# Performance work log

Measured on AMD Instinct MI355X. Metric: run time of the kernel, lower is better.

## Reference

```python
import jax, jax.numpy as jnp
import numpy as np

NB, NX, NY, NU, NQ = 16384, 256, 128, 128, 128


def setup_inputs() -> dict:
    key = jax.random.key(0)
    ks = jax.random.split(key, 14)
    sx = 1.0 / np.sqrt(NX)
    su = 1.0 / np.sqrt(NU)
    sq = 1.0 / np.sqrt(NQ)
    return {
        "x": jax.random.normal(ks[0], (NB, NX), jnp.float32),
        "u": jax.random.normal(ks[1], (NB, NU), jnp.float32),
        "F": jax.random.normal(ks[2], (NX, NX), jnp.float32) * sx,
        "B1": jax.random.normal(ks[3], (NX, NQ), jnp.float32) * sq,
        "B2": jax.random.normal(ks[4], (NX, NU), jnp.float32) * su,
        "C1": jax.random.normal(ks[5], (NQ, NX), jnp.float32) * sx,
        "C2": jax.random.normal(ks[6], (NY, NX), jnp.float32) * sx,
        "D11": jax.random.normal(ks[7], (NQ, NQ), jnp.float32) * sq,
        "D12": jax.random.normal(ks[8], (NQ, NU), jnp.float32) * su,
        "D21": jax.random.normal(ks[9], (NY, NQ), jnp.float32) * sq,
        "D22": jax.random.normal(ks[10], (NY, NU), jnp.float32) * su,
        # E must be invertible (torch code takes torch.inverse(E))
        "E": jnp.eye(NX, dtype=jnp.float32) + 0.1 * sx * jax.random.normal(ks[11], (NX, NX), jnp.float32),
        # Lambda must be nonzero on the diagonal (divided by in the solve)
        "Lambda_vec": 1.0 + jax.random.uniform(ks[12], (NQ, 1), jnp.float32),
        "bv": 0.1 * jax.random.normal(ks[13], (NQ, 1), jnp.float32),
    }


def _solve_w(x, u, C1, D11, D12, Lambda_vec, bv):
    # Sequential forward substitution: v_k = (x@C1[k] + w@D11[k] + u@D12[k] + bv[k]) / Lambda[k,k]
    # w[:,j] for j >= k is zero at step k, so only the strictly-lower part of D11 contributes,
    # exactly matching the torch loop semantics.
    nq = C1.shape[0]
    base = x @ C1.T + u @ D12.T + bv[:, 0]  # (nb, nq), w-independent part
    lam = Lambda_vec[:, 0]                   # (nq,)
    w0 = jnp.zeros((x.shape[0], nq), x.dtype)

    def step(w, k):
        vk = (base[:, k] + w @ D11[k]) / lam[k]  # (nb,)
        return w.at[:, k].set(jnp.tanh(vk)), None

    w, _ = jax.lax.scan(step, w0, jnp.arange(nq))
    return w


def reference(x, u, F, B1, B2, C1, C2, D11, D12, D21, D22, E, Lambda_vec, bv):
    w = _solve_w(x, u, C1, D11, D12, Lambda_vec, bv)
    E_inv = jnp.linalg.inv(E)
    dx = x @ (E_inv @ F).T + w @ (E_inv @ B1).T + u @ (E_inv @ B2).T
    y = x @ C2.T + w @ D21.T + u @ D22.T  # feedthrough=True
    return dx, y
```

## Files before the change

kernel.cpp:

```cpp
#include <hip/hip_runtime.h>
#include <hip/hip_bf16.h>
#include <cstddef>

#define NBATCH 16384
#define NX 256
#define NY 128
#define NU 128
#define NQ 128

#define WS_A2     131072
#define WS_A4     196608
#define WS_P2     327680
#define WS_P4     393216
#define WS_WDX    524288
#define WS_BASE   655360
#define WS_W      2752512
#define WS_WCH    4849664
#define WS_WCL    4947968
#define WS_WBH    5046272
#define WS_WBL    5070848
#define WS_D11S   5095424

typedef __attribute__((ext_vector_type(8))) short bf8_t;
typedef __attribute__((ext_vector_type(4))) float f4_t;

#define C2LOG2E 2.8853900817779268f

__device__ __forceinline__ void gload_lds16(const void* g, void* l) {
  __builtin_amdgcn_global_load_lds(
      (const __attribute__((address_space(1))) unsigned int*)g,
      (__attribute__((address_space(3))) unsigned int*)l, 16, 0, 0);
}

__device__ __forceinline__ void splitbf(float a, unsigned short& h, unsigned short& l) {
  __hip_bfloat16 hb = __float2bfloat16(a);
  float hf = __bfloat162float(hb);
  __hip_bfloat16 lb = __float2bfloat16(a - hf);
  h = __builtin_bit_cast(unsigned short, hb);
  l = __builtin_bit_cast(unsigned short, lb);
}

__global__ __launch_bounds__(256) void k_smallmm(const float* __restrict__ A,
                                                 const float* __restrict__ B,
                                                 const float* __restrict__ X,
                                                 float* __restrict__ C,
                                                 int modeA, int modeB, int modeX) {
  __shared__ float As[32][36];
  __shared__ float Bs[32][36];
  int tid = threadIdx.x;
  int tx = tid & 15, ty = tid >> 4;
  int r0 = blockIdx.x * 32, c0 = blockIdx.y * 32;
  int lr = tid >> 3, lc = (tid & 7) * 4;
  float acc00 = 0.f, acc01 = 0.f, acc10 = 0.f, acc11 = 0.f;
  for (int k0 = 0; k0 < 256; k0 += 32) {
    float4 a4 = *(const float4*)&A[(size_t)(r0 + lr) * 256 + k0 + lc];
    float4 b4 = *(const float4*)&B[(size_t)(k0 + lr) * 256 + c0 + lc];
    if (modeA) {
      float av[4] = {a4.x, a4.y, a4.z, a4.w};
#pragma unroll
      for (int q = 0; q < 4; ++q) {
        float d = (r0 + lr == k0 + lc + q) ? 1.0f : 0.0f;
        av[q] = (modeA == 1) ? d - av[q] : 2.0f * d - av[q];
      }
      a4.x = av[0]; a4.y = av[1]; a4.z = av[2]; a4.w = av[3];
    }
    if (modeB) {
      float bvv[4] = {b4.x, b4.y, b4.z, b4.w};
#pragma unroll
      for (int q = 0; q < 4; ++q) {
        float d = (k0 + lr == c0 + lc + q) ? 1.0f : 0.0f;
        bvv[q] = (modeB == 1) ? d - bvv[q] : 2.0f * d - bvv[q];
      }
      b4.x = bvv[0]; b4.y = bvv[1]; b4.z = bvv[2]; b4.w = bvv[3];
    }
    __syncthreads();
    As[lr][lc+0] = a4.x; As[lr][lc+1] = a4.y; As[lr][lc+2] = a4.z; As[lr][lc+3] = a4.w;
    Bs[lr][lc+0] = b4.x; Bs[lr][lc+1] = b4.y; Bs[lr][lc+2] = b4.z; Bs[lr][lc+3] = b4.w;
    __syncthreads();
#pragma unroll
    for (int kk = 0; kk < 32; ++kk) {
      float a0 = As[ty*2+0][kk], a1 = As[ty*2+1][kk];
      float b0 = Bs[kk][tx*2+0], b1 = Bs[kk][tx*2+1];
      acc00 += a0*b0; acc01 += a0*b1; acc10 += a1*b0; acc11 += a1*b1;
    }
  }
  int r = r0 + ty*2, c = c0 + tx*2;
  if (modeX) {
#pragma unroll
    for (int i = 0; i < 2; ++i)
#pragma unroll
      for (int j = 0; j < 2; ++j) {
        float xv = X[(size_t)(r+i)*256 + c+j];
        float d = (r+i == c+j) ? 1.0f : 0.0f;
        float add = (modeX == 1) ? xv : 2.0f * d - xv;
        if (i==0 && j==0) acc00 += add;
        if (i==0 && j==1) acc01 += add;
        if (i==1 && j==0) acc10 += add;
        if (i==1 && j==1) acc11 += add;
      }
  }
  C[(size_t)r*256 + c]       = acc00; C[(size_t)r*256 + c+1]     = acc01;
  C[(size_t)(r+1)*256 + c]   = acc10; C[(size_t)(r+1)*256 + c+1] = acc11;
}

__global__ __launch_bounds__(256) void k_wdx(const float* __restrict__ P,
                                             const float* __restrict__ F,
                                             const float* __restrict__ B1,
                                             const float* __restrict__ B2,
                                             float* __restrict__ Wdx) {
  __shared__ float As[32][36];
  __shared__ float Bs[32][36];
  int tid = threadIdx.x;
  int tx = tid & 15, ty = tid >> 4;
  int r0 = blockIdx.x * 32, c0 = blockIdx.y * 32;
  const float* B; int ldb, cb;
  if (c0 < 256)      { B = F;  ldb = 256; cb = c0; }
  else if (c0 < 384) { B = B1; ldb = 128; cb = c0 - 256; }
  else               { B = B2; ldb = 128; cb = c0 - 384; }
  int lr = tid >> 3, lc = (tid & 7) * 4;
  float acc00 = 0.f, acc01 = 0.f, acc10 = 0.f, acc11 = 0.f;
  for (int k0 = 0; k0 < 256; k0 += 32) {
    float4 a4 = *(const float4*)&P[(size_t)(r0 + lr) * 256 + k0 + lc];
    float4 b4 = *(const float4*)&B[(size_t)(k0 + lr) * ldb + cb + lc];
    __syncthreads();
    As[lr][lc+0] = a4.x; As[lr][lc+1] = a4.y; As[lr][lc+2] = a4.z; As[lr][lc+3] = a4.w;
    Bs[lr][lc+0] = b4.x; Bs[lr][lc+1] = b4.y; Bs[lr][lc+2] = b4.z; Bs[lr][lc+3] = b4.w;
    __syncthreads();
#pragma unroll
    for (int kk = 0; kk < 32; ++kk) {
      float a0 = As[ty*2+0][kk], a1 = As[ty*2+1][kk];
      float b0 = Bs[kk][tx*2+0], b1 = Bs[kk][tx*2+1];
      acc00 += a0*b0; acc01 += a0*b1; acc10 += a1*b0; acc11 += a1*b1;
    }
  }
  int r = r0 + ty*2, c = c0 + tx*2;
  Wdx[(size_t)r*512 + c]       = acc00; Wdx[(size_t)r*512 + c+1]     = acc01;
  Wdx[(size_t)(r+1)*512 + c]   = acc10; Wdx[(size_t)(r+1)*512 + c+1] = acc11;
}

__global__ __launch_bounds__(256) void k_wprep(const float* __restrict__ Wdx,
                                               const float* __restrict__ C2,
                                               const float* __restrict__ D21,
                                               const float* __restrict__ D22,
                                               const float* __restrict__ C1,
                                               const float* __restrict__ D12,
                                               const float* __restrict__ D11,
                                               const float* __restrict__ Lam,
                                               ushort* __restrict__ Wh,
                                               ushort* __restrict__ Wl,
                                               ushort* __restrict__ Wbh,
                                               ushort* __restrict__ Wbl,
                                               float* __restrict__ D11s) {
  int i = blockIdx.x * 256 + threadIdx.x;
  if (i < 384 * 512) {
    int n = i >> 9, k = i & 511;
    float v;
    if (n < 256) v = Wdx[(size_t)n * 512 + k];
    else {
      int nn = n - 256;
      if (k < 256)      v = C2[(size_t)nn * 256 + k];
      else if (k < 384) v = D21[(size_t)nn * 128 + (k - 256)];
      else              v = D22[(size_t)nn * 128 + (k - 384)];
    }
    unsigned short h, l; splitbf(v, h, l);
    Wh[i] = h; Wl[i] = l;
  } else if (i < 384 * 512 + 128 * 384) {
    int j = i - 384 * 512;
    int n = j / 384, k = j - n * 384;
    float v = (k < 256) ? C1[(size_t)n * 256 + k] : D12[(size_t)n * 128 + (k - 256)];
    unsigned short h, l; splitbf(v, h, l);
    Wbh[j] = h; Wbl[j] = l;
  } else if (i < 384 * 512 + 128 * 384 + 128 * 128) {
    int j2 = i - (384 * 512 + 128 * 384);
    int jr = j2 >> 7;
    D11s[j2] = D11[j2] * (C2LOG2E / Lam[jr]);
  } else if (i < 384 * 512 + 128 * 384 + 128 * 128 + 128) {
    int i3 = i - (384 * 512 + 128 * 384 + 128 * 128);
    D11s[128 * 128 + i3] = C2LOG2E / Lam[i3];
  }
}

template <int KTOT, bool FINAL>
__global__ __launch_bounds__(256) void k_gemm2(const float* __restrict__ x,
                                               const float* __restrict__ u,
                                               const float* __restrict__ w,
                                               const ushort* __restrict__ Wh,
                                               const ushort* __restrict__ Wl,
                                               const float* __restrict__ bv,
                                               float* __restrict__ out) {
  __shared__ __align__(16) ushort sA[128 * 64];
  __shared__ __align__(16) ushort sB[64 * 64];
  const int tid  = threadIdx.x;
  const int lane = tid & 63, wav = tid >> 6;
  const int wm = wav >> 1, wn = wav & 1;
  const int row0 = blockIdx.x * 128;
  const int n0   = blockIdx.y * 64;
  const int fr = lane & 15, fc = lane >> 4;

  const int arow_l = tid >> 3;
  const int akb    = (tid & 7) * 4;

  f4_t acc[4][2];
#pragma unroll
  for (int i = 0; i < 4; ++i)
#pragma unroll
    for (int j = 0; j < 2; ++j) acc[i][j] = f4_t{0.f, 0.f, 0.f, 0.f};

  float4 ar[4];
#define LOAD_A(K0)                                                    \
  {                                                                   \
    int kseg = (K0) + akb;                                            \
    const float* ap0;                                                 \
    _Pragma("unroll")                                                 \
    for (int j = 0; j < 4; ++j) {                                     \
      size_t gr = (size_t)(row0 + j * 32 + arow_l);                   \
      if (FINAL) {                                                    \
        if (kseg < 256)      ap0 = x + gr * 256 + kseg;               \
        else if (kseg < 384) ap0 = w + gr * 128 + (kseg - 256);       \
        else                 ap0 = u + gr * 128 + (kseg - 384);       \
      } else {                                                        \
        if (kseg < 256)      ap0 = x + gr * 256 + kseg;               \
        else                 ap0 = u + gr * 128 + (kseg - 256);       \
      }                                                               \
      ar[j] = *(const float4*)ap0;                                    \
    }                                                                 \
  }

  const int NK = KTOT / 32;
  LOAD_A(0);

  for (int ks = 0; ks < NK; ++ks) {
    const int k0 = ks * 32;
    __syncthreads();

#pragma unroll
    for (int j = 0; j < 4; ++j) {
      int r = j * 32 + arow_l;
      unsigned short h0,l0,h1,l1,h2,l2,h3,l3;
      splitbf(ar[j].x, h0, l0); splitbf(ar[j].y, h1, l1);
      splitbf(ar[j].z, h2, l2); splitbf(ar[j].w, h3, l3);
      uint2 hv, lv;
      hv.x = (unsigned)h0 | ((unsigned)h1 << 16); hv.y = (unsigned)h2 | ((unsigned)h3 << 16);
      lv.x = (unsigned)l0 | ((unsigned)l1 << 16); lv.y = (unsigned)l2 | ((unsigned)l3 << 16);
      int ch   = (tid & 7) >> 1;
      int hoff = (tid & 1) * 8;
      char* rb = (char*)&sA[r * 64];
      *(uint2*)(rb + (((ch    ) ^ (r & 7)) << 4) + hoff) = hv;
      *(uint2*)(rb + (((ch + 4) ^ (r & 7)) << 4) + hoff) = lv;
    }

#pragma unroll
    for (int i = 0; i < 2; ++i) {
      int rbase = wav * 16 + i * 8;
      int nloc  = rbase + (lane >> 3);
      int c     = lane & 7;
      int g     = c ^ (nloc & 7);
      const ushort* src = (g < 4)
          ? (Wh + (size_t)(n0 + nloc) * KTOT + k0 + g * 8)
          : (Wl + (size_t)(n0 + nloc) * KTOT + k0 + (g - 4) * 8);
      gload_lds16(src, &sB[rbase * 64]);
    }

    {
      int kpre = (ks + 1 < NK) ? k0 + 32 : k0;
      LOAD_A(kpre);
    }
    asm volatile("s_waitcnt vmcnt(4)" ::: "memory");
    __syncthreads();

    bf8_t ah[4], al[4], bh[2], bl[2];
#pragma unroll
    for (int ms = 0; ms < 4; ++ms) {
      int r = wm * 64 + ms * 16 + fr;
      char* rb = (char*)&sA[r * 64];
      ah[ms] = *(const bf8_t*)(rb + (((fc    ) ^ (r & 7)) << 4));
      al[ms] = *(const bf8_t*)(rb + (((fc + 4) ^ (r & 7)) << 4));
    }
#pragma unroll
    for (int ns = 0; ns < 2; ++ns) {
      int n = wn * 32 + ns * 16 + fr;
      char* rb = (char*)&sB[n * 64];
      bh[ns] = *(const bf8_t*)(rb + (((fc    ) ^ (n & 7)) << 4));
      bl[ns] = *(const bf8_t*)(rb + (((fc + 4) ^ (n & 7)) << 4));
    }
#pragma unroll
    for (int ns = 0; ns < 2; ++ns)
#pragma unroll
      for (int ms = 0; ms < 4; ++ms) {
        acc[ms][ns] = __builtin_amdgcn_mfma_f32_16x16x32_bf16(ah[ms], bh[ns], acc[ms][ns], 0, 0, 0);
        acc[ms][ns] = __builtin_amdgcn_mfma_f32_16x16x32_bf16(ah[ms], bl[ns], acc[ms][ns], 0, 0, 0);
        acc[ms][ns] = __builtin_amdgcn_mfma_f32_16x16x32_bf16(al[ms], bh[ns], acc[ms][ns], 0, 0, 0);
      }
  }
#undef LOAD_A

#pragma unroll
  for (int ms = 0; ms < 4; ++ms) {
#pragma unroll
    for (int ns = 0; ns < 2; ++ns) {
#pragma unroll
      for (int j = 0; j < 4; ++j) {
        int m = row0 + wm * 64 + ms * 16 + fc * 4 + j;
        int n = n0 + wn * 32 + ns * 16 + fr;
        float v = acc[ms][ns][j];
        if (FINAL) {
          if (n0 < 256) out[(size_t)m * 256 + n] = v;
          else          out[(size_t)NBATCH * 256 + (size_t)m * 128 + (n - 256)] = v;
        } else {
          out[(size_t)m * 128 + n] = v + bv[n];
        }
      }
    }
  }
}

__device__ __forceinline__ float rdlane(float v, int l) {
  return __builtin_bit_cast(float, __builtin_amdgcn_readlane(__builtin_bit_cast(int, v), l));
}

#define WR 4
__global__ __launch_bounds__(256, 4) void k_wsolve(const float* __restrict__ baseo,
                                                   const float* __restrict__ D11s,
                                                   float* __restrict__ wout) {
  int tid = threadIdx.x;
  int lane = tid & 63, wave = tid >> 6;
  size_t rowbase = (size_t)blockIdx.x * (4 * WR) + (size_t)wave * WR;
  const float* drow0 = D11s + (size_t)lane * 128;
  const float* drow1 = D11s + (size_t)(64 + lane) * 128;
  const float* cvec  = D11s + 128 * 128;

  float t0[WR], t1[WR], w0[WR], w1[WR];
  float c0 = cvec[lane];
  float c1 = cvec[64 + lane];
#pragma unroll
  for (int r = 0; r < WR; ++r) {
    t0[r] = baseo[(rowbase + r) * 128 + lane] * c0;
    t1[r] = baseo[(rowbase + r) * 128 + 64 + lane] * c1;
    w0[r] = 0.f; w1[r] = 0.f;
  }
  float d0 = drow0[0];
  float d1 = drow1[0];
  for (int k = 0; k < 64; ++k) {
    int kn = k + 1;
    float nd0 = (kn < 64) ? drow0[kn] : 0.f;
    float nd1 = drow1[kn];
#pragma unroll
    for (int r = 0; r < WR; ++r) {
      float tk = rdlane(t0[r], k);
      float e  = __builtin_amdgcn_exp2f(tk);
      float wk = 1.0f - 2.0f * __builtin_amdgcn_rcpf(e + 1.0f);
      t0[r] += wk * d0;
      t1[r] += wk * d1;
      if (lane == k) w0[r] = wk;
    }
    d0 = nd0; d1 = nd1;
  }
  for (int k = 64; k < 128; ++k) {
    int kn = k + 1;
    float nd1 = (kn < 128) ? drow1[kn] : 0.f;
#pragma unroll
    for (int r = 0; r < WR; ++r) {
      float tk = rdlane(t1[r], k - 64);
      float e  = __builtin_amdgcn_exp2f(tk);
      float wk = 1.0f - 2.0f * __builtin_amdgcn_rcpf(e + 1.0f);
      t1[r] += wk * d1;
      if (lane == (k - 64)) w1[r] = wk;
    }
    d1 = nd1;
  }
#pragma unroll
  for (int r = 0; r < WR; ++r) {
    wout[(rowbase + r) * 128 + lane]      = w0[r];
    wout[(rowbase + r) * 128 + 64 + lane] = w1[r];
  }
}

extern "C" void kernel_launch(void* const* d_in, const int* in_sizes, int n_in,
                              void* d_out, int out_size, void* d_ws, size_t ws_size,
                              hipStream_t stream) {
  (void)in_sizes; (void)n_in; (void)out_size; (void)ws_size;
  const float* x   = (const float*)d_in[0];
  const float* u   = (const float*)d_in[1];
  const float* F   = (const float*)d_in[2];
  const float* B1  = (const float*)d_in[3];
  const float* B2  = (const float*)d_in[4];
  const float* C1  = (const float*)d_in[5];
  const float* C2  = (const float*)d_in[6];
  const float* D11 = (const float*)d_in[7];
  const float* D12 = (const float*)d_in[8];
  const float* D21 = (const float*)d_in[9];
  const float* D22 = (const float*)d_in[10];
  const float* E   = (const float*)d_in[11];
  const float* Lam = (const float*)d_in[12];
  const float* bv  = (const float*)d_in[13];
  float* out = (float*)d_out;
  float* ws  = (float*)d_ws;

  float* A2   = ws + WS_A2;
  float* A4   = ws + WS_A4;
  float* P2   = ws + WS_P2;
  float* P4   = ws + WS_P4;
  float* Wdx  = ws + WS_WDX;
  float* base = ws + WS_BASE;
  float* wbuf = ws + WS_W;
  ushort* Wch = (ushort*)(ws + WS_WCH);
  ushort* Wcl = (ushort*)(ws + WS_WCL);
  ushort* Wbh = (ushort*)(ws + WS_WBH);
  ushort* Wbl = (ushort*)(ws + WS_WBL);
  float* D11s = ws + WS_D11S;

  k_smallmm<<<dim3(8, 8), 256, 0, stream>>>(E,  E,  nullptr, A2, 1, 1, 0);
  k_smallmm<<<dim3(8, 8), 256, 0, stream>>>(E,  A2, E,       P2, 2, 0, 2);
  k_smallmm<<<dim3(8, 8), 256, 0, stream>>>(A2, A2, nullptr, A4, 0, 0, 0);
  k_smallmm<<<dim3(8, 8), 256, 0, stream>>>(P2, A4, P2,      P4, 0, 0, 1);
  k_wdx<<<dim3(8, 16), 256, 0, stream>>>(P4, F, B1, B2, Wdx);
  k_wprep<<<1025, 256, 0, stream>>>(Wdx, C2, D21, D22, C1, D12, D11, Lam,
                                    Wch, Wcl, Wbh, Wbl, D11s);

  k_gemm2<384, false><<<dim3(128, 2), 256, 0, stream>>>(x, u, nullptr, Wbh, Wbl, bv, base);
  k_wsolve<<<1024, 256, 0, stream>>>(base, D11s, wbuf);
  k_gemm2<512, true><<<dim3(128, 6), 256, 0, stream>>>(x, u, wbuf, Wch, Wcl, nullptr, out);
}
```

Baseline: 222.1 us.

## Shrink GEMM tiles, halve wsolve rows per wave, merge independent small matmuls

The split-bf16 GEMM kernels move from 128x64 tiles to 64-row tiles: 64x32 for the base GEMM and 64x64 for the final GEMM. This launches more workgroups to fill the GPU's compute units. The w-solve kernel now handles 2 rows per wave instead of 4 and drops its occupancy hint, which doubles its grid. The two independent 256x256 matmuls in the E-inverse Newton chain are fused into one launch via blockIdx.z. In exchange, smaller tiles reuse less data per block, and fewer rows per wave leave the serial solve with less ILP for hiding latency.

```diff
diff --git a/kernel.cpp b/kernel.cpp
--- a/kernel.cpp
+++ b/kernel.cpp
@@ -40,11 +40,11 @@
   l = __builtin_bit_cast(unsigned short, lb);
 }
 
-__global__ __launch_bounds__(256) void k_smallmm(const float* __restrict__ A,
-                                                 const float* __restrict__ B,
-                                                 const float* __restrict__ X,
-                                                 float* __restrict__ C,
-                                                 int modeA, int modeB, int modeX) {
+__device__ __forceinline__ void smallmm_body(const float* __restrict__ A,
+                                             const float* __restrict__ B,
+                                             const float* __restrict__ X,
+                                             float* __restrict__ C,
+                                             int modeA, int modeB, int modeX) {
   __shared__ float As[32][36];
   __shared__ float Bs[32][36];
   int tid = threadIdx.x;
@@ -101,6 +101,18 @@
   }
   C[(size_t)r*256 + c]       = acc00; C[(size_t)r*256 + c+1]     = acc01;
   C[(size_t)(r+1)*256 + c]   = acc10; C[(size_t)(r+1)*256 + c+1] = acc11;
+}
+
+__global__ __launch_bounds__(256) void k_mm(const float* A, const float* B,
+                                            const float* X, float* C,
+                                            int mA, int mB, int mX) {
+  smallmm_body(A, B, X, C, mA, mB, mX);
+}
+
+__global__ __launch_bounds__(256) void k_mm_dual(const float* E, const float* A2,
+                                                 float* P2, float* A4) {
+  if (blockIdx.z == 0) smallmm_body(E, A2, E, P2, 2, 0, 2);
+  else                 smallmm_body(A2, A2, nullptr, A4, 0, 0, 0);
 }
 
 __global__ __launch_bounds__(256) void k_wdx(const float* __restrict__ P,
@@ -180,50 +192,51 @@
   }
 }
 
-template <int KTOT, bool FINAL>
-__global__ __launch_bounds__(256) void k_gemm2(const float* __restrict__ x,
+template <int KTOT, bool FINAL, int BN>
+__global__ __launch_bounds__(256) void k_gemm3(const float* __restrict__ x,
                                                const float* __restrict__ u,
                                                const float* __restrict__ w,
                                                const ushort* __restrict__ Wh,
                                                const ushort* __restrict__ Wl,
                                                const float* __restrict__ bv,
                                                float* __restrict__ out) {
-  __shared__ __align__(16) ushort sA[128 * 64];
-  __shared__ __align__(16) ushort sB[64 * 64];
+  constexpr int MS = (BN == 64) ? 2 : 1;
+  constexpr int NS = 2;
+  __shared__ __align__(16) ushort sA[64 * 64];
+  __shared__ __align__(16) ushort sB[BN * 64];
   const int tid  = threadIdx.x;
   const int lane = tid & 63, wav = tid >> 6;
-  const int wm = wav >> 1, wn = wav & 1;
-  const int row0 = blockIdx.x * 128;
-  const int n0   = blockIdx.y * 64;
+  const int wrow0 = (BN == 64) ? (wav >> 1) * 32 : wav * 16;
+  const int wcol0 = (BN == 64) ? (wav & 1) * 32 : 0;
+  const int row0 = blockIdx.x * 64;
+  const int n0   = blockIdx.y * BN;
   const int fr = lane & 15, fc = lane >> 4;
 
-  const int arow_l = tid >> 3;
-  const int akb    = (tid & 7) * 4;
-
-  f4_t acc[4][2];
-#pragma unroll
-  for (int i = 0; i < 4; ++i)
-#pragma unroll
-    for (int j = 0; j < 2; ++j) acc[i][j] = f4_t{0.f, 0.f, 0.f, 0.f};
-
-  float4 ar[4];
+  const int arow = tid >> 2;
+  const int ach  = tid & 3;
+
+  f4_t acc[MS][NS];
+#pragma unroll
+  for (int i = 0; i < MS; ++i)
+#pragma unroll
+    for (int j = 0; j < NS; ++j) acc[i][j] = f4_t{0.f, 0.f, 0.f, 0.f};
+
+  float4 ar[2];
 #define LOAD_A(K0)                                                    \
   {                                                                   \
-    int kseg = (K0) + akb;                                            \
+    int kseg = (K0) + ach * 8;                                        \
+    size_t gr = (size_t)(row0 + arow);                                \
     const float* ap0;                                                 \
-    _Pragma("unroll")                                                 \
-    for (int j = 0; j < 4; ++j) {                                     \
-      size_t gr = (size_t)(row0 + j * 32 + arow_l);                   \
-      if (FINAL) {                                                    \
-        if (kseg < 256)      ap0 = x + gr * 256 + kseg;               \
-        else if (kseg < 384) ap0 = w + gr * 128 + (kseg - 256);       \
-        else                 ap0 = u + gr * 128 + (kseg - 384);       \
-      } else {                                                        \
-        if (kseg < 256)      ap0 = x + gr * 256 + kseg;               \
-        else                 ap0 = u + gr * 128 + (kseg - 256);       \
-      }                                                               \
-      ar[j] = *(const float4*)ap0;                                    \
+    if (FINAL) {                                                      \
+      if (kseg < 256)      ap0 = x + gr * 256 + kseg;                 \
+      else if (kseg < 384) ap0 = w + gr * 128 + (kseg - 256);         \
+      else                 ap0 = u + gr * 128 + (kseg - 384);         \
+    } else {                                                          \
+      if (kseg < 256)      ap0 = x + gr * 256 + kseg;                 \
+      else                 ap0 = u + gr * 128 + (kseg - 256);         \
     }                                                                 \
+    ar[0] = *(const float4*)ap0;                                      \
+    ar[1] = *(const float4*)(ap0 + 4);                                \
   }
 
   const int NK = KTOT / 32;
@@ -233,25 +246,29 @@
     const int k0 = ks * 32;
     __syncthreads();
 
-#pragma unroll
-    for (int j = 0; j < 4; ++j) {
-      int r = j * 32 + arow_l;
-      unsigned short h0,l0,h1,l1,h2,l2,h3,l3;
-      splitbf(ar[j].x, h0, l0); splitbf(ar[j].y, h1, l1);
-      splitbf(ar[j].z, h2, l2); splitbf(ar[j].w, h3, l3);
-      uint2 hv, lv;
-      hv.x = (unsigned)h0 | ((unsigned)h1 << 16); hv.y = (unsigned)h2 | ((unsigned)h3 << 16);
-      lv.x = (unsigned)l0 | ((unsigned)l1 << 16); lv.y = (unsigned)l2 | ((unsigned)l3 << 16);
-      int ch   = (tid & 7) >> 1;
-      int hoff = (tid & 1) * 8;
-      char* rb = (char*)&sA[r * 64];
-      *(uint2*)(rb + (((ch    ) ^ (r & 7)) << 4) + hoff) = hv;
-      *(uint2*)(rb + (((ch + 4) ^ (r & 7)) << 4) + hoff) = lv;
-    }
-
-#pragma unroll
-    for (int i = 0; i < 2; ++i) {
-      int rbase = wav * 16 + i * 8;
+    {
+      unsigned short h[8], l[8];
+      splitbf(ar[0].x, h[0], l[0]); splitbf(ar[0].y, h[1], l[1]);
+      splitbf(ar[0].z, h[2], l[2]); splitbf(ar[0].w, h[3], l[3]);
+      splitbf(ar[1].x, h[4], l[4]); splitbf(ar[1].y, h[5], l[5]);
+      splitbf(ar[1].z, h[6], l[6]); splitbf(ar[1].w, h[7], l[7]);
+      uint4 hv, lv;
+      hv.x = (unsigned)h[0] | ((unsigned)h[1] << 16);
+      hv.y = (unsigned)h[2] | ((unsigned)h[3] << 16);
+      hv.z = (unsigned)h[4] | ((unsigned)h[5] << 16);
+      hv.w = (unsigned)h[6] | ((unsigned)h[7] << 16);
+      lv.x = (unsigned)l[0] | ((unsigned)l[1] << 16);
+      lv.y = (unsigned)l[2] | ((unsigned)l[3] << 16);
+      lv.z = (unsigned)l[4] | ((unsigned)l[5] << 16);
+      lv.w = (unsigned)l[6] | ((unsigned)l[7] << 16);
+      char* rb = (char*)&sA[arow * 64];
+      *(uint4*)(rb + (((ach    ) ^ (arow & 7)) << 4)) = hv;
+      *(uint4*)(rb + (((ach + 4) ^ (arow & 7)) << 4)) = lv;
+    }
+
+#pragma unroll
+    for (int i = 0; i < BN / 32; ++i) {
+      int rbase = wav * (BN / 4) + i * 8;
       int nloc  = rbase + (lane >> 3);
       int c     = lane & 7;
       int g     = c ^ (nloc & 7);
@@ -265,28 +282,28 @@
       int kpre = (ks + 1 < NK) ? k0 + 32 : k0;
       LOAD_A(kpre);
     }
-    asm volatile("s_waitcnt vmcnt(4)" ::: "memory");
-    __syncthreads();
-
-    bf8_t ah[4], al[4], bh[2], bl[2];
-#pragma unroll
-    for (int ms = 0; ms < 4; ++ms) {
-      int r = wm * 64 + ms * 16 + fr;
+    asm volatile("s_waitcnt vmcnt(2)" ::: "memory");
+    __syncthreads();
+
+    bf8_t ah[MS], al[MS], bh[NS], bl[NS];
+#pragma unroll
+    for (int ms = 0; ms < MS; ++ms) {
+      int r = wrow0 + ms * 16 + fr;
       char* rb = (char*)&sA[r * 64];
       ah[ms] = *(const bf8_t*)(rb + (((fc    ) ^ (r & 7)) << 4));
       al[ms] = *(const bf8_t*)(rb + (((fc + 4) ^ (r & 7)) << 4));
     }
 #pragma unroll
-    for (int ns = 0; ns < 2; ++ns) {
-      int n = wn * 32 + ns * 16 + fr;
+    for (int ns = 0; ns < NS; ++ns) {
+      int n = wcol0 + ns * 16 + fr;
       char* rb = (char*)&sB[n * 64];
       bh[ns] = *(const bf8_t*)(rb + (((fc    ) ^ (n & 7)) << 4));
       bl[ns] = *(const bf8_t*)(rb + (((fc + 4) ^ (n & 7)) << 4));
     }
 #pragma unroll
-    for (int ns = 0; ns < 2; ++ns)
-#pragma unroll
-      for (int ms = 0; ms < 4; ++ms) {
+    for (int ns = 0; ns < NS; ++ns)
+#pragma unroll
+      for (int ms = 0; ms < MS; ++ms) {
         acc[ms][ns] = __builtin_amdgcn_mfma_f32_16x16x32_bf16(ah[ms], bh[ns], acc[ms][ns], 0, 0, 0);
         acc[ms][ns] = __builtin_amdgcn_mfma_f32_16x16x32_bf16(ah[ms], bl[ns], acc[ms][ns], 0, 0, 0);
         acc[ms][ns] = __builtin_amdgcn_mfma_f32_16x16x32_bf16(al[ms], bh[ns], acc[ms][ns], 0, 0, 0);
@@ -295,13 +312,13 @@
 #undef LOAD_A
 
 #pragma unroll
-  for (int ms = 0; ms < 4; ++ms) {
-#pragma unroll
-    for (int ns = 0; ns < 2; ++ns) {
+  for (int ms = 0; ms < MS; ++ms) {
+#pragma unroll
+    for (int ns = 0; ns < NS; ++ns) {
 #pragma unroll
       for (int j = 0; j < 4; ++j) {
-        int m = row0 + wm * 64 + ms * 16 + fc * 4 + j;
-        int n = n0 + wn * 32 + ns * 16 + fr;
+        int m = row0 + wrow0 + ms * 16 + fc * 4 + j;
+        int n = n0 + wcol0 + ns * 16 + fr;
         float v = acc[ms][ns][j];
         if (FINAL) {
           if (n0 < 256) out[(size_t)m * 256 + n] = v;
@@ -318,10 +335,10 @@
   return __builtin_bit_cast(float, __builtin_amdgcn_readlane(__builtin_bit_cast(int, v), l));
 }
 
-#define WR 4
-__global__ __launch_bounds__(256, 4) void k_wsolve(const float* __restrict__ baseo,
-                                                   const float* __restrict__ D11s,
-                                                   float* __restrict__ wout) {
+#define WR 2
+__global__ __launch_bounds__(256) void k_wsolve(const float* __restrict__ baseo,
+                                                const float* __restrict__ D11s,
+                                                float* __restrict__ wout) {
   int tid = threadIdx.x;
   int lane = tid & 63, wave = tid >> 6;
   size_t rowbase = (size_t)blockIdx.x * (4 * WR) + (size_t)wave * WR;
@@ -409,15 +426,14 @@
   ushort* Wbl = (ushort*)(ws + WS_WBL);
   float* D11s = ws + WS_D11S;
 
-  k_smallmm<<<dim3(8, 8), 256, 0, stream>>>(E,  E,  nullptr, A2, 1, 1, 0);
-  k_smallmm<<<dim3(8, 8), 256, 0, stream>>>(E,  A2, E,       P2, 2, 0, 2);
-  k_smallmm<<<dim3(8, 8), 256, 0, stream>>>(A2, A2, nullptr, A4, 0, 0, 0);
-  k_smallmm<<<dim3(8, 8), 256, 0, stream>>>(P2, A4, P2,      P4, 0, 0, 1);
+  k_mm<<<dim3(8, 8), 256, 0, stream>>>(E, E, nullptr, A2, 1, 1, 0);
+  k_mm_dual<<<dim3(8, 8, 2), 256, 0, stream>>>(E, A2, P2, A4);
+  k_mm<<<dim3(8, 8), 256, 0, stream>>>(P2, A4, P2, P4, 0, 0, 1);
   k_wdx<<<dim3(8, 16), 256, 0, stream>>>(P4, F, B1, B2, Wdx);
   k_wprep<<<1025, 256, 0, stream>>>(Wdx, C2, D21, D22, C1, D12, D11, Lam,
                                     Wch, Wcl, Wbh, Wbl, D11s);
 
-  k_gemm2<384, false><<<dim3(128, 2), 256, 0, stream>>>(x, u, nullptr, Wbh, Wbl, bv, base);
-  k_wsolve<<<1024, 256, 0, stream>>>(base, D11s, wbuf);
-  k_gemm2<512, true><<<dim3(128, 6), 256, 0, stream>>>(x, u, wbuf, Wch, Wcl, nullptr, out);
-}
+  k_gemm3<384, false, 32><<<dim3(256, 4), 256, 0, stream>>>(x, u, nullptr, Wbh, Wbl, bv, base);
+  k_wsolve<<<2048, 256, 0, stream>>>(base, D11s, wbuf);
+  k_gemm3<512, true, 64><<<dim3(256, 6), 256, 0, stream>>>(x, u, wbuf, Wch, Wcl, nullptr, out);
+}
```

Result: slower. 232.3 us (+4.6%).
